# Optimization experiments

Hardware: AMD Instinct MI355X
Metric: run time of the kernel (lower is better)

The kernel has to match this reference:

```python
import jax, jax.numpy as jnp
import numpy as np

N_EMBD = 1024
N_HEAD = 16
HEAD_DIM = N_EMBD // N_HEAD


def setup_inputs() -> dict:
    key = jax.random.key(0)
    ks = jax.random.split(key, 5)
    B, S = 2, 2048
    scale = 0.02
    return {
        "hidden_states": jax.random.normal(ks[0], (B, S, N_EMBD), dtype=jnp.float32),
        "w_attn": jax.random.normal(ks[1], (N_EMBD, 3 * N_EMBD), dtype=jnp.float32) * scale,
        "b_attn": jnp.zeros((3 * N_EMBD,), dtype=jnp.float32),
        "w_proj": jax.random.normal(ks[2], (N_EMBD, N_EMBD), dtype=jnp.float32) * scale,
        "b_proj": jnp.zeros((N_EMBD,), dtype=jnp.float32),
    }


def reference(hidden_states, w_attn, b_attn, w_proj, b_proj):
    B, S, _ = hidden_states.shape
    qkv = hidden_states @ w_attn + b_attn                     # [B,S,3E]
    q, k, v = jnp.split(qkv, 3, axis=-1)                      # each [B,S,E]

    def split_heads(t):  # [B,S,E] -> [B,H,S,D]
        return t.reshape(B, S, N_HEAD, HEAD_DIM).transpose(0, 2, 1, 3)

    q, k, v = split_heads(q), split_heads(k), split_heads(v)

    scores = jnp.einsum("bhqd,bhkd->bhqk", q, k) / np.sqrt(HEAD_DIM).astype(np.float32)
    causal = jnp.tril(jnp.ones((S, S), dtype=bool))
    scores = jnp.where(causal[None, None], scores, jnp.float32(-jnp.inf))
    attn = jax.nn.softmax(scores, axis=-1)                    # [B,H,S,S]
    out = jnp.einsum("bhqk,bhkd->bhqd", attn, v)              # [B,H,S,D]
    out = out.transpose(0, 2, 1, 3).reshape(B, S, N_EMBD)     # merge heads
    out = out @ w_proj + b_proj
    return out
```

## Files before the change

### kernel.cpp

```cpp
#include <hip/hip_runtime.h>
#include <hip/hip_bf16.h>


typedef __attribute__((ext_vector_type(4))) float  float4v;
typedef __attribute__((ext_vector_type(8))) short  short8v;
typedef __attribute__((ext_vector_type(4))) short  short4v;

#define ATT_SCALE 0.18033688011112042f

__device__ __forceinline__ short f2bf(float f) {
  union { float f; unsigned u; } v; v.f = f;
  unsigned r = v.u + 0x7fffu + ((v.u >> 16) & 1u);
  return (short)(r >> 16);
}
__device__ __forceinline__ float bf2f(short s) {
  union { unsigned u; float f; } v; v.u = ((unsigned)(unsigned short)s) << 16;
  return v.f;
}

__device__ __forceinline__ short4v pack_bf16x4(float a, float b, float c, float d) {
  unsigned x0 = __builtin_bit_cast(unsigned, a) + 0x8000u;
  unsigned x1 = __builtin_bit_cast(unsigned, b) + 0x8000u;
  unsigned x2 = __builtin_bit_cast(unsigned, c) + 0x8000u;
  unsigned x3 = __builtin_bit_cast(unsigned, d) + 0x8000u;
  union { unsigned u[2]; short4v s; } r;
  r.u[0] = __builtin_amdgcn_perm(x1, x0, 0x07060302);
  r.u[1] = __builtin_amdgcn_perm(x3, x2, 0x07060302);
  return r.s;
}

__device__ __forceinline__ short4v cvt_pk_bf16x4(float a, float b, float c, float d) {
  union { unsigned u[2]; short4v s; } r;
  asm("v_cvt_pk_bf16_f32 %0, %1, %2" : "=v"(r.u[0]) : "v"(a), "v"(b));
  asm("v_cvt_pk_bf16_f32 %0, %1, %2" : "=v"(r.u[1]) : "v"(c), "v"(d));
  return r.s;
}

__device__ __forceinline__ void gl_lds16(const void* g, void* l) {
  __builtin_amdgcn_global_load_lds(
      (const __attribute__((address_space(1))) unsigned*)g,
      (__attribute__((address_space(3))) unsigned*)l, 16, 0, 0);
}

__global__ __launch_bounds__(256) void prep_kernel(
    const float* __restrict__ hidden, const float* __restrict__ w_attn,
    const float* __restrict__ w_proj, short* __restrict__ hA,
    short* __restrict__ wqkvT, short* __restrict__ wprojT) {
  __shared__ float tile[32][33];
  const int bx = blockIdx.x, t = threadIdx.x;
  if (bx < 4096) {
    const size_t i = ((size_t)bx * 256 + t) * 4;
    float4v v = *(const float4v*)(hidden + i);
    short4v o;
    #pragma unroll
    for (int k = 0; k < 4; k++) o[k] = f2bf(v[k]);
    *(short4v*)(hA + i) = o;
    return;
  }
  const float* in; short* out; int R, C, cx, cy;
  if (bx < 4096 + 3072) {
    in = w_attn; out = wqkvT; R = 1024; C = 3072;
    cx = (bx - 4096) % 96; cy = (bx - 4096) / 96;
  } else {
    in = w_proj; out = wprojT; R = 1024; C = 1024;
    cx = (bx - 7168) % 32; cy = (bx - 7168) / 32;
  }
  const int tx = t & 31, ty = t >> 5;
  const int c0 = cx * 32, r0 = cy * 32;
  #pragma unroll
  for (int i = 0; i < 4; i++)
    tile[ty + i * 8][tx] = in[(size_t)(r0 + ty + i * 8) * C + c0 + tx];
  __syncthreads();
  #pragma unroll
  for (int i = 0; i < 4; i++) {
    const int cc = ty + i * 8;
    out[(size_t)(c0 + cc) * R + r0 + tx] = f2bf(tile[tx][cc]);
  }
}

__global__ __launch_bounds__(512, 2) void gemm_qkv256(
    const short* __restrict__ A, const short* __restrict__ Bt,
    const float* __restrict__ bias, short* __restrict__ qkv,
    short* __restrict__ vA)
{
  __shared__ short As[2][256][64];
  __shared__ short Bs[2][256][64];
  const int K = 1024;
  const int t = threadIdx.x;
  const int lane = t & 63, w = t >> 6;
  const int wm2 = w >> 2, wn4 = w & 3;
  const int l16 = lane & 15, quad = lane >> 4;
  const int e7 = l16 & 7;
  const int row0 = blockIdx.y * 256;
  const int col0 = blockIdx.x * 256;

  float4v acc[8][4] = {};

  const int srow = w * 8 + (lane >> 3);
  const int slog = (lane & 7) ^ (lane >> 3);
  const short* gA = A + (size_t)(row0 + srow) * K + slog * 8;
  const short* gB = Bt + (size_t)(col0 + srow) * K + slog * 8;
  const int sdst = (lane & 7) * 8;

  auto stageA = [&](int b, int qd, int kt) {
    gl_lds16(gA + (size_t)qd * 64 * K + kt * 64,
             &As[b][qd * 64 + w * 8 + (lane >> 3)][sdst]);
  };
  auto stageB = [&](int b, int qd, int kt) {
    gl_lds16(gB + (size_t)qd * 64 * K + kt * 64,
             &Bs[b][qd * 64 + w * 8 + (lane >> 3)][sdst]);
  };

  short8v af[4], bf0[4], bf1[4];
  auto ldA = [&](int b, int mh, int ks) {
    #pragma unroll
    for (int m = 0; m < 4; m++) {
      const int row = wm2 * 128 + mh * 64 + m * 16 + l16;
      af[m] = *(const short8v*)&As[b][row][((ks * 4 + quad) ^ e7) * 8];
    }
  };
  auto ldB = [&](short8v* bf, int b, int ks) {
    #pragma unroll
    for (int n = 0; n < 4; n++) {
      const int row = wn4 * 64 + n * 16 + l16;
      bf[n] = *(const short8v*)&Bs[b][row][((ks * 4 + quad) ^ e7) * 8];
    }
  };
  auto mm = [&](int mb, short8v* bf) {
    __builtin_amdgcn_s_setprio(1);
    #pragma unroll
    for (int m = 0; m < 4; m++)
      #pragma unroll
      for (int n = 0; n < 4; n++)
        acc[mb + m][n] =
            __builtin_amdgcn_mfma_f32_16x16x32_bf16(af[m], bf[n], acc[mb + m][n], 0, 0, 0);
    __builtin_amdgcn_s_setprio(0);
  };
  auto sync_mfma = [&]() {
    __builtin_amdgcn_sched_barrier(0);
    __builtin_amdgcn_s_barrier();
    asm volatile("s_waitcnt lgkmcnt(0)" ::: "memory");
    __builtin_amdgcn_sched_barrier(0);
  };
  auto endp = [&]() {
    __builtin_amdgcn_sched_barrier(0);
    __builtin_amdgcn_s_barrier();
    __builtin_amdgcn_sched_barrier(0);
  };

  #pragma unroll
  for (int qd = 0; qd < 4; qd++) stageA(0, qd, 0);
  #pragma unroll
  for (int qd = 0; qd < 4; qd++) stageB(0, qd, 0);
  #pragma unroll
  for (int qd = 0; qd < 4; qd++) stageB(1, qd, 1);
  asm volatile("s_waitcnt vmcnt(4)" ::: "memory");
  __builtin_amdgcn_s_barrier();
  __builtin_amdgcn_sched_barrier(0);

  const int NIT = K / 128;
  #pragma unroll 1
  for (int it = 0; it < NIT; it++) {
    const bool st = (it < NIT - 1);
    const int t1 = 2 * it + 1, t2 = 2 * it + 2, t3 = 2 * it + 3;

    ldA(0, 0, 0); ldB(bf0, 0, 0);
    stageA(1, 0, t1); stageA(1, 1, t1);
    sync_mfma(); mm(0, bf0); endp();
    ldA(0, 0, 1); ldB(bf1, 0, 1);
    stageA(1, 2, t1); stageA(1, 3, t1);
    sync_mfma(); mm(0, bf1); endp();
    ldA(0, 1, 0);
    if (st) { stageB(0, 0, t2); stageB(0, 1, t2); }
    sync_mfma(); mm(4, bf0); endp();
    ldA(0, 1, 1);
    if (st) { stageB(0, 2, t2); stageB(0, 3, t2); }
    if (st) asm volatile("s_waitcnt vmcnt(4)" ::: "memory");
    else    asm volatile("s_waitcnt vmcnt(0)" ::: "memory");
    sync_mfma(); mm(4, bf1); endp();

    ldA(1, 0, 0); ldB(bf0, 1, 0);
    if (st) { stageA(0, 0, t2); stageA(0, 1, t2); }
    sync_mfma(); mm(0, bf0); endp();
    ldA(1, 0, 1); ldB(bf1, 1, 1);
    if (st) { stageA(0, 2, t2); stageA(0, 3, t2); }
    sync_mfma(); mm(0, bf1); endp();
    ldA(1, 1, 0);
    if (st) { stageB(1, 0, t3); stageB(1, 1, t3); }
    sync_mfma(); mm(4, bf0); endp();
    ldA(1, 1, 1);
    if (st) { stageB(1, 2, t3); stageB(1, 3, t3); }
    if (st) asm volatile("s_waitcnt vmcnt(4)" ::: "memory");
    sync_mfma(); mm(4, bf1); endp();
  }

  if (col0 >= 2048) {
    const int b  = row0 >> 11;
    const int hh = ((col0 - 2048) >> 6) + wn4;
    #pragma unroll
    for (int ktl = 0; ktl < 2; ktl++) {
      const int kt = ((row0 & 2047) >> 6) + wm2 * 2 + ktl;
      short* vbase = vA + ((size_t)((b * 16 + hh) * 32 + kt) * 8) * 512;
      #pragma unroll
      for (int j = 0; j < 4; j++) {
        const float bv = bias[col0 + wn4 * 64 + j * 16 + l16];
        #pragma unroll
        for (int kwp = 0; kwp < 2; kwp++) {
          short8v s8;
          #pragma unroll
          for (int kw = 0; kw < 2; kw++) {
            const int mi = ktl * 4 + kwp * 2 + kw;
            short4v q4 = pack_bf16x4(acc[mi][j][0] + bv, acc[mi][j][1] + bv,
                                     acc[mi][j][2] + bv, acc[mi][j][3] + bv);
            #pragma unroll
            for (int r = 0; r < 4; r++) s8[kw * 4 + r] = q4[r];
          }
          *(short8v*)(vbase + ((size_t)(kwp * 4 + j) * 64 + lane) * 8) = s8;
        }
      }
    }
    return;
  }
  #pragma unroll
  for (int j = 0; j < 4; j++) {
    const int col = col0 + wn4 * 64 + j * 16 + l16;
    const float sc = (col < 1024) ? ATT_SCALE : 1.0f;
    const float bv = bias[col];
    #pragma unroll
    for (int mi = 0; mi < 8; mi++) {
      #pragma unroll
      for (int r = 0; r < 4; r++) {
        const int row = row0 + wm2 * 128 + mi * 16 + quad * 4 + r;
        qkv[(size_t)row * 3072 + col] = f2bf((acc[mi][j][r] + bv) * sc);
      }
    }
  }
}

template<int RB, int MODE>
__global__ __launch_bounds__(256) void gemm_bt(
    const short* __restrict__ A, const short* __restrict__ Bt,
    const float* __restrict__ bias, void* __restrict__ Cout,
    short* __restrict__ vA, int M, int N, int K)
{
  __shared__ short As[3][RB][32];
  __shared__ short Bs[3][128][32];
  const int MI = RB / 32;
  const int t    = threadIdx.x;
  const int lane = t & 63;
  const int wave = t >> 6;
  const int wm   = (wave >> 1) * (RB / 2);
  const int wn   = (wave & 1) * 64;
  const int l16  = lane & 15;
  const int quad = lane >> 4;
  const int row0 = blockIdx.y * RB;
  const int col0 = blockIdx.x * 128;

  float4v acc[MI][4] = {};

  const int srow = lane >> 2;
  const int scol = (lane & 3) * 8;
  const int gcol = ((lane & 3) ^ ((srow >> 1) & 3)) * 8;
  const int rquad = (quad ^ ((l16 >> 1) & 3)) * 8;

  const short* gA0 = A + (size_t)(row0 + wave * ((RB == 128) ? 32 : 16) + srow) * K + gcol;
  const short* gA1 = gA0 + (size_t)16 * K;
  const short* gB0 = Bt + (size_t)(col0 + wave * 32 + srow) * K + gcol;
  const short* gB1 = gB0 + (size_t)16 * K;

  const int NI = K / 32;

  auto stage = [&](int kt, int b) {
    const int k0 = kt * 32;
    if (RB == 128) {
      gl_lds16(gA0 + k0, &As[b][wave * 32 + srow][scol]);
      gl_lds16(gA1 + k0, &As[b][wave * 32 + 16 + srow][scol]);
    } else {
      gl_lds16(gA0 + k0, &As[b][(wave * 16 + srow) & (RB - 1)][scol]);
    }
    gl_lds16(gB0 + k0, &Bs[b][wave * 32 + srow][scol]);
    gl_lds16(gB1 + k0, &Bs[b][wave * 32 + 16 + srow][scol]);
  };

  stage(0, 0);
  stage(1, 1);
  if (RB == 128) asm volatile("s_waitcnt vmcnt(4)" ::: "memory");
  else           asm volatile("s_waitcnt vmcnt(3)" ::: "memory");
  __builtin_amdgcn_s_barrier();
  __builtin_amdgcn_sched_barrier(0);

  int buf = 0;
  for (int i = 0; i < NI; i++) {
    if (i + 2 < NI) stage(i + 2, (buf + 2 >= 3) ? buf - 1 : buf + 2);

    short8v af[MI], bf[4];
    #pragma unroll
    for (int ii = 0; ii < MI; ii++)
      af[ii] = *(const short8v*)&As[buf][wm + ii * 16 + l16][rquad];
    #pragma unroll
    for (int j = 0; j < 4; j++)
      bf[j] = *(const short8v*)&Bs[buf][wn + j * 16 + l16][rquad];
    #pragma unroll
    for (int ii = 0; ii < MI; ii++)
      #pragma unroll
      for (int j = 0; j < 4; j++)
        acc[ii][j] = __builtin_amdgcn_mfma_f32_16x16x32_bf16(af[ii], bf[j], acc[ii][j], 0, 0, 0);

    if (i + 1 < NI) {
      if (i + 2 < NI) {
        if (RB == 128) asm volatile("s_waitcnt vmcnt(4)" ::: "memory");
        else           asm volatile("s_waitcnt vmcnt(3)" ::: "memory");
      } else {
        asm volatile("s_waitcnt vmcnt(0)" ::: "memory");
      }
      __builtin_amdgcn_s_barrier();
      __builtin_amdgcn_sched_barrier(0);
    }
    buf = (buf >= 2) ? 0 : buf + 1;
  }

  #pragma unroll
  for (int j = 0; j < 4; j++) {
    const int col = col0 + wn + j * 16 + l16;
    const float bv = bias[col];
    #pragma unroll
    for (int i = 0; i < MI; i++) {
      #pragma unroll
      for (int r = 0; r < 4; r++) {
        const int row = row0 + wm + i * 16 + quad * 4 + r;
        ((float*)Cout)[(size_t)row * N + col] = acc[i][j][r] + bv;
      }
    }
  }
}

__global__ __launch_bounds__(256, 4) void attn_mfma(
    const short* __restrict__ qkv, const short* __restrict__ vA,
    short* __restrict__ P0, short* __restrict__ P1, float* __restrict__ lp)
{
  __shared__ short KA[2][8 * 512];

  const int bh = blockIdx.x;
  const int b = bh >> 4, h = bh & 15;
  const int s = 79 - blockIdx.y;
  int qt = 0, sbase = 0;
  for (;;) { const int nc = (qt >> 3) + 1; if (s < sbase + nc) break; sbase += nc; qt++; }
  const int c = s - sbase;
  const int kt0  = c * 8;
  const int kend = min(qt + 1, kt0 + 8);

  const int t = threadIdx.x;
  const int lane = t & 63, w = t >> 6;
  const int l16 = lane & 15, quad = lane >> 4;

  const size_t base = (size_t)b * 2048 * 3072;
  const int qoff = h * 64, koff = 1024 + h * 64;
  const int qg = qt * 64 + w * 16 + l16;

  short8v qf[2];
  #pragma unroll
  for (int ks = 0; ks < 2; ks++)
    qf[ks] = *(const short8v*)(qkv + base + (size_t)qg * 3072 + qoff + ks * 32 + quad * 8);

  float4v O[4] = {};
  float l = 0.0f;

  const int id0 = w * 2, id1 = id0 + 1;
  const int jm0 = id0 & 3, ks0 = id0 >> 2;
  const int jm1 = id1 & 3, ks1 = id1 >> 2;
  const short* kg0 = qkv + base + (size_t)(jm0 * 16 + l16) * 3072 + koff + ks0 * 32 + quad * 8;
  const short* kg1 = qkv + base + (size_t)(jm1 * 16 + l16) * 3072 + koff + ks1 * 32 + quad * 8;
  const short* vg  = vA + (size_t)(bh * 32) * 4096 + lane * 8;

  gl_lds16(kg0 + (size_t)kt0 * 64 * 3072, &KA[0][id0 * 512 + lane * 8]);
  gl_lds16(kg1 + (size_t)kt0 * 64 * 3072, &KA[0][id1 * 512 + lane * 8]);

  for (int kt = kt0; kt < kend; kt++) {
    const int buf = (kt - kt0) & 1;
    __syncthreads();

    short8v vv[8];
    #pragma unroll
    for (int id = 0; id < 8; id++)
      vv[id] = *(const short8v*)(vg + (size_t)kt * 4096 + id * 512);

    if (kt + 1 < kend) {
      gl_lds16(kg0 + (size_t)(kt + 1) * 64 * 3072, &KA[buf ^ 1][id0 * 512 + lane * 8]);
      gl_lds16(kg1 + (size_t)(kt + 1) * 64 * 3072, &KA[buf ^ 1][id1 * 512 + lane * 8]);
    }

    float4v sv[4] = {};
    __builtin_amdgcn_s_setprio(1);
    #pragma unroll
    for (int ks = 0; ks < 2; ks++)
      #pragma unroll
      for (int jm = 0; jm < 4; jm++) {
        const short8v kf = *(const short8v*)&KA[buf][(ks * 4 + jm) * 512 + lane * 8];
        sv[jm] = __builtin_amdgcn_mfma_f32_16x16x32_bf16(kf, qf[ks], sv[jm], 0, 0, 0);
      }
    __builtin_amdgcn_s_setprio(0);

    if (kt == qt) {
      #pragma unroll
      for (int jm = 0; jm < 4; jm++) {
        const int kv = kt * 64 + jm * 16 + quad * 4;
        #pragma unroll
        for (int r = 0; r < 4; r++)
          if (kv + r > qg) sv[jm][r] = -INFINITY;
      }
    }

    short4v pk[4];
    #pragma unroll
    for (int jm = 0; jm < 4; jm++) {
      float p0 = __builtin_amdgcn_exp2f(sv[jm][0]);
      float p1 = __builtin_amdgcn_exp2f(sv[jm][1]);
      float p2 = __builtin_amdgcn_exp2f(sv[jm][2]);
      float p3 = __builtin_amdgcn_exp2f(sv[jm][3]);
      l += (p0 + p1) + (p2 + p3);
      pk[jm] = cvt_pk_bf16x4(p0, p1, p2, p3);
    }

    __builtin_amdgcn_s_setprio(1);
    #pragma unroll
    for (int id = 0; id < 8; id++) {
      const int kwp = id >> 2, dm = id & 3;
      const short8v v8 = vv[id];
      const short4v v0 = {v8[0], v8[1], v8[2], v8[3]};
      const short4v v1 = {v8[4], v8[5], v8[6], v8[7]};
      O[dm] = __builtin_amdgcn_mfma_f32_16x16x16bf16_1k(v0, pk[kwp * 2],     O[dm], 0, 0, 0);
      O[dm] = __builtin_amdgcn_mfma_f32_16x16x16bf16_1k(v1, pk[kwp * 2 + 1], O[dm], 0, 0, 0);
    }
    __builtin_amdgcn_s_setprio(0);
  }

  l += __shfl_xor(l, 16);
  l += __shfl_xor(l, 32);
  const int i = bh * 80 + s;
  short* pp = (i < 2048) ? (P0 + (size_t)i * 4096) : (P1 + (size_t)(i - 2048) * 4096);
  const int row = w * 16 + l16;
  if (quad == 0) lp[(size_t)i * 64 + row] = l;
  short* pr = pp + row * 64;
  #pragma unroll
  for (int dm = 0; dm < 4; dm++)
    *(short4v*)(pr + dm * 16 + quad * 4) =
        pack_bf16x4(O[dm][0], O[dm][1], O[dm][2], O[dm][3]);
}

__global__ __launch_bounds__(256) void merge_attn(
    const short* __restrict__ P0, const short* __restrict__ P1,
    const float* __restrict__ lp, short* __restrict__ aout)
{
  const int idx = blockIdx.x * 256 + threadIdx.x;
  const int q = idx >> 7;
  const int rest = idx & 127;
  const int h  = rest >> 3;
  const int dg = (rest & 7) * 8;
  const int b  = q >> 11;
  const int qr = q & 2047;
  const int qt = qr >> 6;
  const int row = qr & 63;
  const int a = qt >> 3, bq = qt & 7;
  const int off = qt + 4 * a * (a - 1) + a * bq;
  const int nc  = a + 1;
  const int bh  = b * 16 + h;

  float acc[8] = {};
  float suml = 0.0f;
  for (int c = 0; c < nc; c++) {
    const int i = bh * 80 + off + c;
    const short* pp = (i < 2048) ? (P0 + (size_t)i * 4096) : (P1 + (size_t)(i - 2048) * 4096);
    const short8v o = *(const short8v*)(pp + row * 64 + dg);
    #pragma unroll
    for (int k = 0; k < 8; k++) acc[k] += bf2f(o[k]);
    suml += lp[(size_t)i * 64 + row];
  }
  const float inv = 1.0f / suml;
  short8v ov;
  #pragma unroll
  for (int k = 0; k < 8; k++) ov[k] = f2bf(acc[k] * inv);
  *(short8v*)(aout + (size_t)q * 1024 + h * 64 + dg) = ov;
}

extern "C" void kernel_launch(void* const* d_in, const int* in_sizes, int n_in,
                              void* d_out, int out_size, void* d_ws, size_t ws_size,
                              hipStream_t stream) {
  const float* hidden = (const float*)d_in[0];
  const float* w_attn = (const float*)d_in[1];
  const float* b_attn = (const float*)d_in[2];
  const float* w_proj = (const float*)d_in[3];
  const float* b_proj = (const float*)d_in[4];
  float* outp = (float*)d_out;

  char* ws = (char*)d_ws;
  short* hA     = (short*)(ws);
  float* lp     = (float*)(ws + 8ull  * 1024 * 1024);
  short* wqkvT  = (short*)(ws + 8ull  * 1024 * 1024);
  short* wprojT = (short*)(ws + 14ull * 1024 * 1024);
  short* qkvb   = (short*)(ws + 16ull * 1024 * 1024);
  short* vAbuf  = (short*)(ws + 40ull * 1024 * 1024);
  short* aout   = (short*)(ws + 40ull * 1024 * 1024);
  short* P0     = (short*)d_out;

  prep_kernel<<<8192, 256, 0, stream>>>(hidden, w_attn, w_proj, hA, wqkvT, wprojT);
  gemm_qkv256<<<dim3(12, 16), 512, 0, stream>>>(hA, wqkvT, b_attn, qkvb, vAbuf);
  attn_mfma<<<dim3(32, 80), 256, 0, stream>>>(qkvb, vAbuf, P0, hA, lp);
  merge_attn<<<2048, 256, 0, stream>>>(P0, hA, lp, aout);
  gemm_bt<64, 0><<<dim3(8, 64), 256, 0, stream>>>(aout, wprojT, b_proj, outp, nullptr, 4096, 1024, 1024);
}
```

Baseline: 189.5 us.

## Stage K tiles in pairs to halve barriers in attention loop

The attention kernel's K staging moves from one tile per iteration to a pair of tiles per iteration. Two tiles are prefetched into a ping-pong buffer, and each __syncthreads now covers two compute steps. This halves block barriers per KV tile and issues prefetches earlier, at the cost of double the LDS for K (16KB to 32KB), which may reduce occupancy at 4 blocks per CU.

Result: no change. 192.2 us (+1.4%).

```diff
diff --git a/kernel.cpp b/kernel.cpp
--- a/kernel.cpp
+++ b/kernel.cpp
@@ -338,7 +338,7 @@
     const short* __restrict__ qkv, const short* __restrict__ vA,
     short* __restrict__ P0, short* __restrict__ P1, float* __restrict__ lp)
 {
-  __shared__ short KA[2][8 * 512];
+  __shared__ short KA[2][2][8 * 512];
 
   const int bh = blockIdx.x;
   const int b = bh >> 4, h = bh & 15;
@@ -372,22 +372,16 @@
   const short* kg1 = qkv + base + (size_t)(jm1 * 16 + l16) * 3072 + koff + ks1 * 32 + quad * 8;
   const short* vg  = vA + (size_t)(bh * 32) * 4096 + lane * 8;
 
-  gl_lds16(kg0 + (size_t)kt0 * 64 * 3072, &KA[0][id0 * 512 + lane * 8]);
-  gl_lds16(kg1 + (size_t)kt0 * 64 * 3072, &KA[0][id1 * 512 + lane * 8]);
-
-  for (int kt = kt0; kt < kend; kt++) {
-    const int buf = (kt - kt0) & 1;
-    __syncthreads();
-
+  auto stageK = [&](int kt, int pb, int slot) {
+    gl_lds16(kg0 + (size_t)kt * 64 * 3072, &KA[pb][slot][id0 * 512 + lane * 8]);
+    gl_lds16(kg1 + (size_t)kt * 64 * 3072, &KA[pb][slot][id1 * 512 + lane * 8]);
+  };
+
+  auto tile_compute = [&](int pb, int slot, int ktc) {
     short8v vv[8];
     #pragma unroll
     for (int id = 0; id < 8; id++)
-      vv[id] = *(const short8v*)(vg + (size_t)kt * 4096 + id * 512);
-
-    if (kt + 1 < kend) {
-      gl_lds16(kg0 + (size_t)(kt + 1) * 64 * 3072, &KA[buf ^ 1][id0 * 512 + lane * 8]);
-      gl_lds16(kg1 + (size_t)(kt + 1) * 64 * 3072, &KA[buf ^ 1][id1 * 512 + lane * 8]);
-    }
+      vv[id] = *(const short8v*)(vg + (size_t)ktc * 4096 + id * 512);
 
     float4v sv[4] = {};
     __builtin_amdgcn_s_setprio(1);
@@ -395,15 +389,15 @@
     for (int ks = 0; ks < 2; ks++)
       #pragma unroll
       for (int jm = 0; jm < 4; jm++) {
-        const short8v kf = *(const short8v*)&KA[buf][(ks * 4 + jm) * 512 + lane * 8];
+        const short8v kf = *(const short8v*)&KA[pb][slot][(ks * 4 + jm) * 512 + lane * 8];
         sv[jm] = __builtin_amdgcn_mfma_f32_16x16x32_bf16(kf, qf[ks], sv[jm], 0, 0, 0);
       }
     __builtin_amdgcn_s_setprio(0);
 
-    if (kt == qt) {
+    if (ktc == qt) {
       #pragma unroll
       for (int jm = 0; jm < 4; jm++) {
-        const int kv = kt * 64 + jm * 16 + quad * 4;
+        const int kv = ktc * 64 + jm * 16 + quad * 4;
         #pragma unroll
         for (int r = 0; r < 4; r++)
           if (kv + r > qg) sv[jm][r] = -INFINITY;
@@ -432,6 +426,23 @@
       O[dm] = __builtin_amdgcn_mfma_f32_16x16x16bf16_1k(v1, pk[kwp * 2 + 1], O[dm], 0, 0, 0);
     }
     __builtin_amdgcn_s_setprio(0);
+  };
+
+  stageK(kt0, 0, 0);
+  if (kt0 + 1 < kend) stageK(kt0 + 1, 0, 1);
+
+  int kt = kt0;
+  for (;;) {
+    const int pb = ((kt - kt0) >> 1) & 1;
+    __syncthreads();
+    if (kt + 2 < kend) {
+      stageK(kt + 2, pb ^ 1, 0);
+      if (kt + 3 < kend) stageK(kt + 3, pb ^ 1, 1);
+    }
+    tile_compute(pb, 0, kt);
+    if (++kt == kend) break;
+    tile_compute(pb, 1, kt);
+    if (++kt == kend) break;
   }
 
   l += __shfl_xor(l, 16);
```

## Process two 16-row query slices per wave in attention, halving block size

Applied to the files above, without the earlier changes.

The attention kernel now runs 2 waves (128 threads) per block instead of 4, with each wave handling 32 query rows (two 16-row slices). Each K fragment read from LDS and each V fragment loaded from global memory now feeds two MFMAs, and each wave stages four K chunks instead of two. This cuts the LDS and global loads of K and V per unit of MFMA work. In exchange it uses more registers per wave and leaves fewer waves per block to hide latency.

New measurement: 184.3 us. 1.03x faster.

```diff
diff --git a/kernel.cpp b/kernel.cpp
--- a/kernel.cpp
+++ b/kernel.cpp
@@ -334,7 +334,7 @@
   }
 }
 
-__global__ __launch_bounds__(256, 4) void attn_mfma(
+__global__ __launch_bounds__(128, 3) void attn_mfma(
     const short* __restrict__ qkv, const short* __restrict__ vA,
     short* __restrict__ P0, short* __restrict__ P1, float* __restrict__ lp)
 {
@@ -355,25 +355,32 @@
 
   const size_t base = (size_t)b * 2048 * 3072;
   const int qoff = h * 64, koff = 1024 + h * 64;
-  const int qg = qt * 64 + w * 16 + l16;
-
-  short8v qf[2];
-  #pragma unroll
-  for (int ks = 0; ks < 2; ks++)
-    qf[ks] = *(const short8v*)(qkv + base + (size_t)qg * 3072 + qoff + ks * 32 + quad * 8);
-
-  float4v O[4] = {};
-  float l = 0.0f;
-
-  const int id0 = w * 2, id1 = id0 + 1;
-  const int jm0 = id0 & 3, ks0 = id0 >> 2;
-  const int jm1 = id1 & 3, ks1 = id1 >> 2;
-  const short* kg0 = qkv + base + (size_t)(jm0 * 16 + l16) * 3072 + koff + ks0 * 32 + quad * 8;
-  const short* kg1 = qkv + base + (size_t)(jm1 * 16 + l16) * 3072 + koff + ks1 * 32 + quad * 8;
+
+  int qg[2];
+  short8v qf[2][2];
+  #pragma unroll
+  for (int hh = 0; hh < 2; hh++) {
+    qg[hh] = qt * 64 + w * 32 + hh * 16 + l16;
+    #pragma unroll
+    for (int ks = 0; ks < 2; ks++)
+      qf[hh][ks] = *(const short8v*)(qkv + base + (size_t)qg[hh] * 3072
+                                     + qoff + ks * 32 + quad * 8);
+  }
+
+  float4v O[2][4] = {};
+  float l[2] = {0.0f, 0.0f};
+
+  const short* kgw = qkv + base + (size_t)l16 * 3072 + koff + w * 32 + quad * 8;
   const short* vg  = vA + (size_t)(bh * 32) * 4096 + lane * 8;
 
-  gl_lds16(kg0 + (size_t)kt0 * 64 * 3072, &KA[0][id0 * 512 + lane * 8]);
-  gl_lds16(kg1 + (size_t)kt0 * 64 * 3072, &KA[0][id1 * 512 + lane * 8]);
+  auto stageK = [&](int kt, int buf) {
+    #pragma unroll
+    for (int j = 0; j < 4; j++)
+      gl_lds16(kgw + ((size_t)kt * 64 + j * 16) * 3072,
+               &KA[buf][(w * 4 + j) * 512 + lane * 8]);
+  };
+
+  stageK(kt0, 0);
 
   for (int kt = kt0; kt < kend; kt++) {
     const int buf = (kt - kt0) & 1;
@@ -384,42 +391,46 @@
     for (int id = 0; id < 8; id++)
       vv[id] = *(const short8v*)(vg + (size_t)kt * 4096 + id * 512);
 
-    if (kt + 1 < kend) {
-      gl_lds16(kg0 + (size_t)(kt + 1) * 64 * 3072, &KA[buf ^ 1][id0 * 512 + lane * 8]);
-      gl_lds16(kg1 + (size_t)(kt + 1) * 64 * 3072, &KA[buf ^ 1][id1 * 512 + lane * 8]);
-    }
-
-    float4v sv[4] = {};
+    if (kt + 1 < kend) stageK(kt + 1, buf ^ 1);
+
+    float4v sv[2][4] = {};
     __builtin_amdgcn_s_setprio(1);
     #pragma unroll
     for (int ks = 0; ks < 2; ks++)
       #pragma unroll
       for (int jm = 0; jm < 4; jm++) {
         const short8v kf = *(const short8v*)&KA[buf][(ks * 4 + jm) * 512 + lane * 8];
-        sv[jm] = __builtin_amdgcn_mfma_f32_16x16x32_bf16(kf, qf[ks], sv[jm], 0, 0, 0);
+        #pragma unroll
+        for (int hh = 0; hh < 2; hh++)
+          sv[hh][jm] = __builtin_amdgcn_mfma_f32_16x16x32_bf16(kf, qf[hh][ks],
+                                                               sv[hh][jm], 0, 0, 0);
       }
     __builtin_amdgcn_s_setprio(0);
 
     if (kt == qt) {
       #pragma unroll
+      for (int hh = 0; hh < 2; hh++)
+        #pragma unroll
+        for (int jm = 0; jm < 4; jm++) {
+          const int kv = kt * 64 + jm * 16 + quad * 4;
+          #pragma unroll
+          for (int r = 0; r < 4; r++)
+            if (kv + r > qg[hh]) sv[hh][jm][r] = -INFINITY;
+        }
+    }
+
+    short4v pk[2][4];
+    #pragma unroll
+    for (int hh = 0; hh < 2; hh++)
+      #pragma unroll
       for (int jm = 0; jm < 4; jm++) {
-        const int kv = kt * 64 + jm * 16 + quad * 4;
-        #pragma unroll
-        for (int r = 0; r < 4; r++)
-          if (kv + r > qg) sv[jm][r] = -INFINITY;
-      }
-    }
-
-    short4v pk[4];
-    #pragma unroll
-    for (int jm = 0; jm < 4; jm++) {
-      float p0 = __builtin_amdgcn_exp2f(sv[jm][0]);
-      float p1 = __builtin_amdgcn_exp2f(sv[jm][1]);
-      float p2 = __builtin_amdgcn_exp2f(sv[jm][2]);
-      float p3 = __builtin_amdgcn_exp2f(sv[jm][3]);
-      l += (p0 + p1) + (p2 + p3);
-      pk[jm] = cvt_pk_bf16x4(p0, p1, p2, p3);
-    }
+        float p0 = __builtin_amdgcn_exp2f(sv[hh][jm][0]);
+        float p1 = __builtin_amdgcn_exp2f(sv[hh][jm][1]);
+        float p2 = __builtin_amdgcn_exp2f(sv[hh][jm][2]);
+        float p3 = __builtin_amdgcn_exp2f(sv[hh][jm][3]);
+        l[hh] += (p0 + p1) + (p2 + p3);
+        pk[hh][jm] = cvt_pk_bf16x4(p0, p1, p2, p3);
+      }
 
     __builtin_amdgcn_s_setprio(1);
     #pragma unroll
@@ -428,23 +439,34 @@
       const short8v v8 = vv[id];
       const short4v v0 = {v8[0], v8[1], v8[2], v8[3]};
       const short4v v1 = {v8[4], v8[5], v8[6], v8[7]};
-      O[dm] = __builtin_amdgcn_mfma_f32_16x16x16bf16_1k(v0, pk[kwp * 2],     O[dm], 0, 0, 0);
-      O[dm] = __builtin_amdgcn_mfma_f32_16x16x16bf16_1k(v1, pk[kwp * 2 + 1], O[dm], 0, 0, 0);
+      #pragma unroll
+      for (int hh = 0; hh < 2; hh++) {
+        O[hh][dm] = __builtin_amdgcn_mfma_f32_16x16x16bf16_1k(v0, pk[hh][kwp * 2],
+                                                              O[hh][dm], 0, 0, 0);
+        O[hh][dm] = __builtin_amdgcn_mfma_f32_16x16x16bf16_1k(v1, pk[hh][kwp * 2 + 1],
+                                                              O[hh][dm], 0, 0, 0);
+      }
     }
     __builtin_amdgcn_s_setprio(0);
   }
 
-  l += __shfl_xor(l, 16);
-  l += __shfl_xor(l, 32);
+  #pragma unroll
+  for (int hh = 0; hh < 2; hh++) {
+    l[hh] += __shfl_xor(l[hh], 16);
+    l[hh] += __shfl_xor(l[hh], 32);
+  }
   const int i = bh * 80 + s;
   short* pp = (i < 2048) ? (P0 + (size_t)i * 4096) : (P1 + (size_t)(i - 2048) * 4096);
-  const int row = w * 16 + l16;
-  if (quad == 0) lp[(size_t)i * 64 + row] = l;
-  short* pr = pp + row * 64;
-  #pragma unroll
-  for (int dm = 0; dm < 4; dm++)
-    *(short4v*)(pr + dm * 16 + quad * 4) =
-        pack_bf16x4(O[dm][0], O[dm][1], O[dm][2], O[dm][3]);
+  #pragma unroll
+  for (int hh = 0; hh < 2; hh++) {
+    const int row = w * 32 + hh * 16 + l16;
+    if (quad == 0) lp[(size_t)i * 64 + row] = l[hh];
+    short* pr = pp + row * 64;
+    #pragma unroll
+    for (int dm = 0; dm < 4; dm++)
+      *(short4v*)(pr + dm * 16 + quad * 4) =
+          pack_bf16x4(O[hh][dm][0], O[hh][dm][1], O[hh][dm][2], O[hh][dm][3]);
+  }
 }
 
 __global__ __launch_bounds__(256) void merge_attn(
@@ -504,7 +526,7 @@
 
   prep_kernel<<<8192, 256, 0, stream>>>(hidden, w_attn, w_proj, hA, wqkvT, wprojT);
   gemm_qkv256<<<dim3(12, 16), 512, 0, stream>>>(hA, wqkvT, b_attn, qkvb, vAbuf);
-  attn_mfma<<<dim3(32, 80), 256, 0, stream>>>(qkvb, vAbuf, P0, hA, lp);
+  attn_mfma<<<dim3(32, 80), 128, 0, stream>>>(qkvb, vAbuf, P0, hA, lp);
   merge_attn<<<2048, 256, 0, stream>>>(P0, hA, lp, aout);
   gemm_bt<64, 0><<<dim3(8, 64), 256, 0, stream>>>(aout, wprojT, b_proj, outp, nullptr, 4096, 1024, 1024);
 }
```
